# Kernel tuning notes

Hardware: AMD Instinct MI355X
Metric: run time of the kernel (lower is better)

The kernel has to match this reference:

```python
import jax, jax.numpy as jnp
import numpy as np

EPS = 1e-6
BASE_THETA = 10000.0


def setup_inputs() -> dict:
    key = jax.random.key(0)
    ks = jax.random.split(key, 6)
    S, E = 4096, 4096
    scale = 1.0 / np.sqrt(E)
    return {
        "x": jax.random.normal(ks[0], (S, E), dtype=jnp.float32),
        "w_q": jax.random.normal(ks[1], (E, E), dtype=jnp.float32) * scale,
        "w_k": jax.random.normal(ks[2], (E, E), dtype=jnp.float32) * scale,
        "w_v": jax.random.normal(ks[3], (E, E), dtype=jnp.float32) * scale,
        "w_out": jax.random.normal(ks[4], (E, E), dtype=jnp.float32) * scale,
        "scaling_factor": jax.random.uniform(ks[5], (E,), dtype=jnp.float32, minval=0.5, maxval=1.5),
    }


def _rope_apply(t, cos, sin):
    # t: (S, D) fp16; cos/sin: (S, D//2) fp16. Closed form of the per-position
    # block-diagonal 2x2 rotation matrix matmul in the original loop:
    # out[2j]   =  t[2j]*cos + t[2j+1]*sin
    # out[2j+1] = -t[2j]*sin + t[2j+1]*cos
    S, D = t.shape
    t2 = t.reshape(S, D // 2, 2)
    even, odd = t2[..., 0], t2[..., 1]
    out = jnp.stack([even * cos + odd * sin, -even * sin + odd * cos], axis=-1)
    return out.reshape(S, D)


def reference(x, w_q, w_k, w_v, w_out, scaling_factor):
    f16, f32 = jnp.float16, jnp.float32
    S, E = x.shape
    # __init__: q / q_inv / head rotations are identity; quantize = cast fp16 (scale 1).
    # q_inv * scaling_factor.view(1,-1) == diag(scaling_factor) -> row-scale weights.
    wq = (scaling_factor[:, None] * w_q).astype(f16)
    wk = (scaling_factor[:, None] * w_k).astype(f16)
    wv = (scaling_factor[:, None] * w_v).astype(f16)
    wo = w_out.astype(f16)

    # input @ identity; rms_norm in fp32
    xn = x * jax.lax.rsqrt(jnp.mean(x * x, axis=-1, keepdims=True) + EPS)
    xq = xn.astype(f16)

    # quantized matmuls: fp16 operands, fp32 accumulation, cast back to fp16
    q = (xq.astype(f32) @ wq.astype(f32)).astype(f16)
    k = (xq.astype(f32) @ wk.astype(f32)).astype(f16)
    v = (xq.astype(f32) @ wv.astype(f32)).astype(f16)

    # RoPE over full feature dim (size = E), vectorized over positions
    pos = jnp.arange(S, dtype=f32)[:, None]
    j = jnp.arange(E // 2, dtype=f32)[None, :]
    theta = pos / jnp.power(BASE_THETA, 2.0 * j / E)
    cos = jnp.cos(theta).astype(f16)
    sin = jnp.sin(theta).astype(f16)
    q = _rope_apply(q, cos, sin)
    k = _rope_apply(k, cos, sin)

    # rot_head_k_tiled is identity -> quantize is just fp16 cast (already fp16)
    scores = (q.astype(f32) @ k.T.astype(f32)).astype(f16)
    scores = scores / np.float16(np.sqrt(E))
    # causal mask: strict upper triangle -> -inf
    row = jnp.arange(S)[:, None]
    col = jnp.arange(S)[None, :]
    scores = jnp.where(col > row, jnp.float16(-jnp.inf), scores)
    attn_w = jax.nn.softmax(scores, axis=1)
    attn = attn_w @ v  # fp16 matmul as in original

    out = (attn.astype(f32) @ wo.astype(f32)).astype(f16)
    return out
```

## Files before the change

kernel.cpp:

```cpp
#include <hip/hip_runtime.h>
#include <hip/hip_bf16.h>
#include <cmath>


typedef _Float16 f16;
typedef _Float16 f16x4 __attribute__((ext_vector_type(4)));
typedef _Float16 f16x8 __attribute__((ext_vector_type(8)));
typedef float f32x4 __attribute__((ext_vector_type(4)));

#define S_DIM 4096
#define E_DIM 4096

__device__ __forceinline__ void gload_lds16(const void* g, void* l) {
  __builtin_amdgcn_global_load_lds((const __attribute__((address_space(1))) void*)g,
                                   (__attribute__((address_space(3))) void*)l,
                                   16, 0, 0);
}

__global__ __launch_bounds__(256) void rmsnorm_f16(const float* __restrict__ x,
                                                   f16* __restrict__ xq,
                                                   float* __restrict__ ftab,
                                                   int E) {
  const int row = blockIdx.x;
  const int t = threadIdx.x;
  if (row < 8) {
    const int j = row * 256 + t;
    ftab[j] = (float)pow(10000.0, (double)j / 2048.0);
  }
  const float4* xr = (const float4*)(x + (size_t)row * E);
  float4 v[4];
  float ss = 0.f;
#pragma unroll
  for (int i = 0; i < 4; ++i) {
    v[i] = xr[t + 256 * i];
    ss += v[i].x * v[i].x + v[i].y * v[i].y + v[i].z * v[i].z + v[i].w * v[i].w;
  }
#pragma unroll
  for (int o = 1; o < 64; o <<= 1) ss += __shfl_xor(ss, o);
  __shared__ float red[4];
  const int wid = t >> 6, lane = t & 63;
  if (lane == 0) red[wid] = ss;
  __syncthreads();
  const float tot = red[0] + red[1] + red[2] + red[3];
  const float r = 1.0f / sqrtf(tot / (float)E + 1e-6f);
  f16* xo = xq + (size_t)row * E;
#pragma unroll
  for (int i = 0; i < 4; ++i) {
    f16x4 o;
    o[0] = (f16)(v[i].x * r);
    o[1] = (f16)(v[i].y * r);
    o[2] = (f16)(v[i].z * r);
    o[3] = (f16)(v[i].w * r);
    *(f16x4*)(xo + 4 * (t + 256 * i)) = o;
  }
}

__global__ __launch_bounds__(256) void wconv_t(const float* __restrict__ W,
                                               const float* __restrict__ s,
                                               f16* __restrict__ WT, int N) {
  __shared__ f16 tile[64][65];
  const int tr = blockIdx.y * 64;
  const int tc = blockIdx.x * 64;
  const int t = threadIdx.x;
  const int r = t / 16;
  const int c4 = (t % 16) * 4;
#pragma unroll
  for (int i = 0; i < 4; ++i) {
    const int row = r + i * 16;
    float4 w = *(const float4*)(W + (size_t)(tr + row) * N + tc + c4);
    const float sc = s ? s[tr + row] : 1.0f;
    tile[row][c4 + 0] = (f16)(w.x * sc);
    tile[row][c4 + 1] = (f16)(w.y * sc);
    tile[row][c4 + 2] = (f16)(w.z * sc);
    tile[row][c4 + 3] = (f16)(w.w * sc);
  }
  __syncthreads();
#pragma unroll
  for (int i = 0; i < 4; ++i) {
    const int row = r + i * 16;
    f16x4 o;
    o[0] = tile[c4 + 0][row];
    o[1] = tile[c4 + 1][row];
    o[2] = tile[c4 + 2][row];
    o[3] = tile[c4 + 3][row];
    *(f16x4*)(WT + (size_t)(tc + row) * N + tr + c4) = o;
  }
}

__global__ __launch_bounds__(256) void rope_qk(f16* __restrict__ q,
                                               f16* __restrict__ k,
                                               const float* __restrict__ ftab,
                                               int E) {
  const int idx = blockIdx.x * 256 + threadIdx.x;
  const int cpr = E / 8;
  const int pos = idx / cpr;
  const int ch = idx % cpr;
  const int j0 = ch * 4;
  const float fpos = (float)pos;
  f16x8 qv = *(f16x8*)(q + (size_t)idx * 8);
  f16x8 kv = *(f16x8*)(k + (size_t)idx * 8);
  f16x8 qo, ko;
#pragma unroll
  for (int p = 0; p < 4; ++p) {
    const int j = j0 + p;
    const float th = fpos / ftab[j];
    float sn, cs;
    sincosf(th, &sn, &cs);
    const f16 c16 = (f16)cs, s16 = (f16)sn;
    const float c = (float)c16, s = (float)s16;
    {
      const float e = (float)qv[2 * p], o = (float)qv[2 * p + 1];
      const f16 t1 = (f16)(e * c), t2 = (f16)(o * s);
      const f16 u1 = (f16)(-(e * s)), u2 = (f16)(o * c);
      qo[2 * p] = (f16)((float)t1 + (float)t2);
      qo[2 * p + 1] = (f16)((float)u1 + (float)u2);
    }
    {
      const float e = (float)kv[2 * p], o = (float)kv[2 * p + 1];
      const f16 t1 = (f16)(e * c), t2 = (f16)(o * s);
      const f16 u1 = (f16)(-(e * s)), u2 = (f16)(o * c);
      ko[2 * p] = (f16)((float)t1 + (float)t2);
      ko[2 * p + 1] = (f16)((float)u1 + (float)u2);
    }
  }
  *(f16x8*)(q + (size_t)idx * 8) = qo;
  *(f16x8*)(k + (size_t)idx * 8) = ko;
}

__global__ __launch_bounds__(256) void softmax_causal(f16* __restrict__ sc, int S) {
  const int row = blockIdx.x;
  const int t = threadIdx.x;
  f16* p = sc + (size_t)row * S;
  const int cend = (row & ~255) + 256;
  float v[16];
  bool msk[16];
  bool act[2];
#pragma unroll
  for (int i = 0; i < 2; ++i) {
    act[i] = ((i * 256 + t) * 8) < cend;
    if (act[i]) {
      f16x8 a = *(const f16x8*)(p + (size_t)(i * 256 + t) * 8);
#pragma unroll
      for (int j = 0; j < 8; ++j) v[i * 8 + j] = (float)a[j];
    }
  }
  float m = -1e30f;
#pragma unroll
  for (int i = 0; i < 2; ++i)
    if (act[i])
#pragma unroll
      for (int j = 0; j < 8; ++j) {
        const int col = (i * 256 + t) * 8 + j;
        const int ii = i * 8 + j;
        msk[ii] = (col > row);
        if (!msk[ii]) m = fmaxf(m, v[ii]);
      }
#pragma unroll
  for (int o = 1; o < 64; o <<= 1) m = fmaxf(m, __shfl_xor(m, o));
  __shared__ float red[4];
  const int wid = t >> 6, lane = t & 63;
  if (lane == 0) red[wid] = m;
  __syncthreads();
  m = fmaxf(fmaxf(red[0], red[1]), fmaxf(red[2], red[3]));
  __syncthreads();
  f16 e16[16];
  float sum = 0.f;
#pragma unroll
  for (int i = 0; i < 2; ++i)
    if (act[i])
#pragma unroll
      for (int j = 0; j < 8; ++j) {
        const int ii = i * 8 + j;
        if (msk[ii]) {
          e16[ii] = (f16)0.0f;
        } else {
          const f16 d16 = (f16)(v[ii] - m);
          e16[ii] = (f16)expf((float)d16);
          sum += (float)e16[ii];
        }
      }
#pragma unroll
  for (int o = 1; o < 64; o <<= 1) sum += __shfl_xor(sum, o);
  if (lane == 0) red[wid] = sum;
  __syncthreads();
  sum = red[0] + red[1] + red[2] + red[3];
  const f16 den16 = (f16)sum;
  const float den = (float)den16;
#pragma unroll
  for (int i = 0; i < 2; ++i) {
    if (!act[i]) continue;
    f16x8 o;
#pragma unroll
    for (int j = 0; j < 8; ++j) {
      const int ii = i * 8 + j;
      o[j] = msk[ii] ? (f16)0.0f : (f16)((float)e16[ii] / den);
    }
    *(f16x8*)(p + (size_t)(i * 256 + t) * 8) = o;
  }
}

__device__ __forceinline__ void store_out(f16* p, f16 v) { *p = v; }
__device__ __forceinline__ void store_out(float* p, f16 v) { *p = (float)v; }

template <typename OUT, int MODE>
__global__ __launch_bounds__(512, 2) void gemm256(const f16* __restrict__ A,
                                                  const f16* __restrict__ BT,
                                                  OUT* __restrict__ C,
                                                  int M, int N, int K, float alpha) {
  if (MODE == 1 && blockIdx.x > blockIdx.y) return;
  const int bm = blockIdx.y * 256, bn = blockIdx.x * 256;
  const int kend = (MODE == 2) ? (bm + 256 < K ? bm + 256 : K) : K;
  const int nt = kend >> 6;

  extern __shared__ char smem[];
  f16(*lds)[2][256][64] = (f16(*)[2][256][64])smem;

  const int tid = threadIdx.x;
  const int lane = tid & 63;
  const int wid = tid >> 6;
  const int wr = wid >> 2;
  const int wc = wid & 3;
  const f16* Ab = A + (size_t)bm * K;
  const f16* Bb = BT + (size_t)bn * K;

  const int l8 = lane >> 3;
  const int gxor8 = ((lane & 7) ^ l8) * 8;
  const int lr = lane & 15;
  const int shi = lane >> 4;
  const int rsw = lr & 7;

  auto STAGE_P = [&](int p) {
    const int c = p + 6;
    const int Ts = c >> 2, hh = c & 3;
    if (Ts >= nt) return;
    const int k0 = Ts << 6;
    const int bsel = Ts & 1;
#pragma unroll
    for (int l = 0; l < 2; ++l) {
      const int rih0 = wid * 16 + l * 8;
      if (hh == 0 || hh == 3) {
        const int row0 = (rih0 & 63) + ((rih0 >> 6) << 7) + ((hh == 3) ? 64 : 0);
        gload_lds16(Ab + (size_t)(row0 + l8) * K + k0 + gxor8,
                    &lds[bsel][0][row0][0]);
      } else {
        const int row0 = (rih0 & 31) + ((rih0 >> 5) << 6) + ((hh == 2) ? 32 : 0);
        gload_lds16(Bb + (size_t)(row0 + l8) * K + k0 + gxor8,
                    &lds[bsel][1][row0][0]);
      }
    }
  };

  f32x4 acc[8][4] = {};
  f16x8 afr0[4][2], afr1[4][2], b0r[2][2], b1r[2][2];

#pragma unroll
  for (int p = -6; p < 0; ++p) STAGE_P(p);

  for (int T = 0; T < nt; ++T) {
    const int cur = T & 1;
    __builtin_amdgcn_sched_barrier(0);
    if (T + 1 < nt) {
      asm volatile("s_waitcnt vmcnt(4)" ::: "memory");
    } else {
      asm volatile("s_waitcnt vmcnt(0)" ::: "memory");
    }
    __builtin_amdgcn_sched_barrier(0);
    __builtin_amdgcn_s_barrier();
    __builtin_amdgcn_sched_barrier(0);
#pragma unroll
    for (int m2 = 0; m2 < 4; ++m2)
#pragma unroll
      for (int kk = 0; kk < 2; ++kk)
        afr0[m2][kk] = *(const f16x8*)&lds[cur][0][wr * 128 + m2 * 16 + lr]
                                          [((kk * 4 + shi) ^ rsw) * 8];
#pragma unroll
    for (int n2 = 0; n2 < 2; ++n2)
#pragma unroll
      for (int kk = 0; kk < 2; ++kk)
        b0r[n2][kk] = *(const f16x8*)&lds[cur][1][wc * 64 + n2 * 16 + lr]
                                         [((kk * 4 + shi) ^ rsw) * 8];
    STAGE_P(4 * T);
    __builtin_amdgcn_sched_barrier(0);
    if (T > 0) {
#pragma unroll
      for (int m2 = 0; m2 < 4; ++m2)
#pragma unroll
        for (int n2 = 0; n2 < 2; ++n2)
#pragma unroll
          for (int kk = 0; kk < 2; ++kk)
            acc[4 + m2][2 + n2] = __builtin_amdgcn_mfma_f32_16x16x32_f16(
                afr1[m2][kk], b1r[n2][kk], acc[4 + m2][2 + n2], 0, 0, 0);
    }
    __builtin_amdgcn_sched_barrier(0);
#pragma unroll
    for (int n2 = 0; n2 < 2; ++n2)
#pragma unroll
      for (int kk = 0; kk < 2; ++kk)
        b1r[n2][kk] = *(const f16x8*)&lds[cur][1][wc * 64 + 32 + n2 * 16 + lr]
                                         [((kk * 4 + shi) ^ rsw) * 8];
    STAGE_P(4 * T + 1);
    __builtin_amdgcn_sched_barrier(0);
#pragma unroll
    for (int m2 = 0; m2 < 4; ++m2)
#pragma unroll
      for (int n2 = 0; n2 < 2; ++n2)
#pragma unroll
        for (int kk = 0; kk < 2; ++kk)
          acc[m2][n2] = __builtin_amdgcn_mfma_f32_16x16x32_f16(
              afr0[m2][kk], b0r[n2][kk], acc[m2][n2], 0, 0, 0);
    __builtin_amdgcn_sched_barrier(0);
    __builtin_amdgcn_s_barrier();
    __builtin_amdgcn_sched_barrier(0);
#pragma unroll
    for (int m2 = 0; m2 < 4; ++m2)
#pragma unroll
      for (int kk = 0; kk < 2; ++kk)
        afr1[m2][kk] = *(const f16x8*)&lds[cur][0][wr * 128 + 64 + m2 * 16 + lr]
                                          [((kk * 4 + shi) ^ rsw) * 8];
    STAGE_P(4 * T + 2);
    __builtin_amdgcn_sched_barrier(0);
#pragma unroll
    for (int m2 = 0; m2 < 4; ++m2)
#pragma unroll
      for (int n2 = 0; n2 < 2; ++n2)
#pragma unroll
        for (int kk = 0; kk < 2; ++kk)
          acc[m2][2 + n2] = __builtin_amdgcn_mfma_f32_16x16x32_f16(
              afr0[m2][kk], b1r[n2][kk], acc[m2][2 + n2], 0, 0, 0);
    __builtin_amdgcn_sched_barrier(0);
    STAGE_P(4 * T + 3);
    __builtin_amdgcn_sched_barrier(0);
#pragma unroll
    for (int m2 = 0; m2 < 4; ++m2)
#pragma unroll
      for (int n2 = 0; n2 < 2; ++n2)
#pragma unroll
        for (int kk = 0; kk < 2; ++kk)
          acc[4 + m2][n2] = __builtin_amdgcn_mfma_f32_16x16x32_f16(
              afr1[m2][kk], b0r[n2][kk], acc[4 + m2][n2], 0, 0, 0);
  }
#pragma unroll
  for (int m2 = 0; m2 < 4; ++m2)
#pragma unroll
    for (int n2 = 0; n2 < 2; ++n2)
#pragma unroll
      for (int kk = 0; kk < 2; ++kk)
        acc[4 + m2][2 + n2] = __builtin_amdgcn_mfma_f32_16x16x32_f16(
            afr1[m2][kk], b1r[n2][kk], acc[4 + m2][2 + n2], 0, 0, 0);

  const int rb_l = wr * 128 + (lane >> 4) * 4;
  const int cb_l = wc * 64 + (lane & 15);

#pragma unroll
  for (int mm = 0; mm < 8; ++mm)
#pragma unroll
    for (int nn = 0; nn < 4; ++nn) {
      const int col = bn + cb_l + nn * 16;
#pragma unroll
      for (int r = 0; r < 4; ++r) {
        f16 h = (f16)acc[mm][nn][r];
        if (alpha != 1.0f) h = (f16)((float)h * alpha);
        store_out(&C[(size_t)(bm + rb_l + mm * 16 + r) * N + col], h);
      }
    }
}

extern "C" void kernel_launch(void* const* d_in, const int* in_sizes, int n_in,
                              void* d_out, int out_size, void* d_ws, size_t ws_size,
                              hipStream_t stream) {
  const float* x = (const float*)d_in[0];
  const float* wq = (const float*)d_in[1];
  const float* wk = (const float*)d_in[2];
  const float* wv = (const float*)d_in[3];
  const float* wo = (const float*)d_in[4];
  const float* sf = (const float*)d_in[5];
  float* out = (float*)d_out;

  const int S = S_DIM, E = E_DIM;
  const size_t U = (size_t)S * E * sizeof(f16);
  char* ws = (char*)d_ws;
  f16* xq = (f16*)(ws + 0 * U);
  f16* wT = (f16*)(ws + 1 * U);
  f16* q  = (f16*)(ws + 2 * U);
  f16* k  = (f16*)(ws + 3 * U);
  f16* vT = (f16*)d_out;
  float* ftab = out + 12 * 1024 * 1024;

  const int LDSA = 131072;
  hipFuncSetAttribute(reinterpret_cast<const void*>(&gemm256<f16, 0>),
                      hipFuncAttributeMaxDynamicSharedMemorySize, LDSA);
  hipFuncSetAttribute(reinterpret_cast<const void*>(&gemm256<f16, 1>),
                      hipFuncAttributeMaxDynamicSharedMemorySize, LDSA);
  hipFuncSetAttribute(reinterpret_cast<const void*>(&gemm256<f16, 2>),
                      hipFuncAttributeMaxDynamicSharedMemorySize, LDSA);
  hipFuncSetAttribute(reinterpret_cast<const void*>(&gemm256<float, 0>),
                      hipFuncAttributeMaxDynamicSharedMemorySize, LDSA);

  dim3 b256(256), b512(512);
  dim3 gT(E / 64, E / 64);
  dim3 gG(E / 256, S / 256);

  rmsnorm_f16<<<S, b256, 0, stream>>>(x, xq, ftab, E);

  wconv_t<<<gT, b256, 0, stream>>>(wq, sf, wT, E);
  gemm256<f16, 0><<<gG, b512, LDSA, stream>>>(xq, wT, q, S, E, E, 1.0f);
  wconv_t<<<gT, b256, 0, stream>>>(wk, sf, wT, E);
  gemm256<f16, 0><<<gG, b512, LDSA, stream>>>(xq, wT, k, S, E, E, 1.0f);
  wconv_t<<<gT, b256, 0, stream>>>(wv, sf, wT, E);
  gemm256<f16, 0><<<dim3(S / 256, E / 256), b512, LDSA, stream>>>(wT, xq, vT,
                                                                  E, S, E, 1.0f);

  rope_qk<<<(S * (E / 8)) / 256, b256, 0, stream>>>(q, k, ftab, E);

  f16* sc = wT;
  gemm256<f16, 1><<<dim3(S / 256, S / 256), b512, LDSA, stream>>>(q, k, sc, S, S,
                                                                  E, 1.0f / 64.0f);
  softmax_causal<<<S, b256, 0, stream>>>(sc, S);

  f16* attn = q;
  gemm256<f16, 2><<<gG, b512, LDSA, stream>>>(sc, vT, attn, S, E, S, 1.0f);

  f16* wT2 = k;
  wconv_t<<<gT, b256, 0, stream>>>(wo, (const float*)nullptr, wT2, E);
  gemm256<float, 0><<<gG, b512, LDSA, stream>>>(attn, wT2, out, S, E, E, 1.0f);
}
```

Measured before the change: 779.3 us.

## Use 128x128 tile GEMM kernel for causal QK^T and PV matmuls

Adds a simpler 128x128-tile GEMM kernel with 256 threads and static LDS, and uses it for the causal score GEMM and the attention-times-V GEMM. The causal block-skipping and K-truncation now operate at 128 granularity, and the softmax column bound is tightened to match. This trims wasted work above the diagonal and improves tile-count balance. The trade-off is that the new kernel is single-buffered with less data reuse than the tuned 256 kernel.

```diff
diff --git a/kernel.cpp b/kernel.cpp
--- a/kernel.cpp
+++ b/kernel.cpp
@@ -131,7 +131,7 @@
   const int row = blockIdx.x;
   const int t = threadIdx.x;
   f16* p = sc + (size_t)row * S;
-  const int cend = (row & ~255) + 256;
+  const int cend = (row & ~127) + 128;
   float v[16];
   bool msk[16];
   bool act[2];
@@ -202,15 +202,82 @@
 __device__ __forceinline__ void store_out(f16* p, f16 v) { *p = v; }
 __device__ __forceinline__ void store_out(float* p, f16 v) { *p = (float)v; }
 
-template <typename OUT, int MODE>
+template <int MODE>
+__global__ __launch_bounds__(256) void gemm128(const f16* __restrict__ A,
+                                               const f16* __restrict__ BT,
+                                               f16* __restrict__ C,
+                                               int M, int N, int K, float alpha) {
+  const int bm = blockIdx.y * 128, bn = blockIdx.x * 128;
+  if (MODE == 1 && bn > bm) return;
+  const int kend = (MODE == 2) ? (bm + 128 < K ? bm + 128 : K) : K;
+
+  __shared__ f16 As[128][64];
+  __shared__ f16 Bs[128][64];
+  const int t = threadIdx.x;
+  const int lane = t & 63;
+  const int wid = t >> 6;
+  const int wr = wid >> 1, wc = wid & 1;
+
+  const int lr = lane & 15;
+  const int shi = lane >> 4;
+  const int rx = lr & 7;
+  const int grow = wid * 8 + (lane >> 3);
+  const int gcol = (((lane & 7) ^ ((lane >> 3) & 7)) * 8);
+
+  f32x4 acc[4][4] = {};
+
+  for (int k0 = 0; k0 < kend; k0 += 64) {
+    __syncthreads();
+#pragma unroll
+    for (int i = 0; i < 4; ++i) {
+      gload_lds16(A + (size_t)(bm + i * 32 + grow) * K + k0 + gcol,
+                  &As[i * 32 + wid * 8][0]);
+      gload_lds16(BT + (size_t)(bn + i * 32 + grow) * K + k0 + gcol,
+                  &Bs[i * 32 + wid * 8][0]);
+    }
+    __syncthreads();
+#pragma unroll
+    for (int kk = 0; kk < 2; ++kk) {
+      const int roff = ((kk * 4 + shi) ^ rx) * 8;
+      f16x8 af[4], bf[4];
+#pragma unroll
+      for (int m = 0; m < 4; ++m)
+        af[m] = *(const f16x8*)&As[wr * 64 + m * 16 + lr][roff];
+#pragma unroll
+      for (int n = 0; n < 4; ++n)
+        bf[n] = *(const f16x8*)&Bs[wc * 64 + n * 16 + lr][roff];
+#pragma unroll
+      for (int m = 0; m < 4; ++m)
+#pragma unroll
+        for (int n = 0; n < 4; ++n)
+          acc[m][n] =
+              __builtin_amdgcn_mfma_f32_16x16x32_f16(af[m], bf[n], acc[m][n], 0, 0, 0);
+    }
+  }
+
+  const int rb = bm + wr * 64 + (lane >> 4) * 4;
+  const int cb = bn + wc * 64 + (lane & 15);
+#pragma unroll
+  for (int m = 0; m < 4; ++m)
+#pragma unroll
+    for (int n = 0; n < 4; ++n) {
+      const int col = cb + n * 16;
+#pragma unroll
+      for (int r = 0; r < 4; ++r) {
+        f16 h = (f16)acc[m][n][r];
+        if (alpha != 1.0f) h = (f16)((float)h * alpha);
+        store_out(&C[(size_t)(rb + m * 16 + r) * N + col], h);
+      }
+    }
+}
+
+template <typename OUT>
 __global__ __launch_bounds__(512, 2) void gemm256(const f16* __restrict__ A,
                                                   const f16* __restrict__ BT,
                                                   OUT* __restrict__ C,
                                                   int M, int N, int K, float alpha) {
-  if (MODE == 1 && blockIdx.x > blockIdx.y) return;
   const int bm = blockIdx.y * 256, bn = blockIdx.x * 256;
-  const int kend = (MODE == 2) ? (bm + 256 < K ? bm + 256 : K) : K;
-  const int nt = kend >> 6;
+  const int nt = K >> 6;
 
   extern __shared__ char smem[];
   f16(*lds)[2][256][64] = (f16(*)[2][256][64])smem;
@@ -387,13 +454,9 @@
   float* ftab = out + 12 * 1024 * 1024;
 
   const int LDSA = 131072;
-  hipFuncSetAttribute(reinterpret_cast<const void*>(&gemm256<f16, 0>),
+  hipFuncSetAttribute(reinterpret_cast<const void*>(&gemm256<f16>),
                       hipFuncAttributeMaxDynamicSharedMemorySize, LDSA);
-  hipFuncSetAttribute(reinterpret_cast<const void*>(&gemm256<f16, 1>),
-                      hipFuncAttributeMaxDynamicSharedMemorySize, LDSA);
-  hipFuncSetAttribute(reinterpret_cast<const void*>(&gemm256<f16, 2>),
-                      hipFuncAttributeMaxDynamicSharedMemorySize, LDSA);
-  hipFuncSetAttribute(reinterpret_cast<const void*>(&gemm256<float, 0>),
+  hipFuncSetAttribute(reinterpret_cast<const void*>(&gemm256<float>),
                       hipFuncAttributeMaxDynamicSharedMemorySize, LDSA);
 
   dim3 b256(256), b512(512);
@@ -403,24 +466,25 @@
   rmsnorm_f16<<<S, b256, 0, stream>>>(x, xq, ftab, E);
 
   wconv_t<<<gT, b256, 0, stream>>>(wq, sf, wT, E);
-  gemm256<f16, 0><<<gG, b512, LDSA, stream>>>(xq, wT, q, S, E, E, 1.0f);
+  gemm256<f16><<<gG, b512, LDSA, stream>>>(xq, wT, q, S, E, E, 1.0f);
   wconv_t<<<gT, b256, 0, stream>>>(wk, sf, wT, E);
-  gemm256<f16, 0><<<gG, b512, LDSA, stream>>>(xq, wT, k, S, E, E, 1.0f);
+  gemm256<f16><<<gG, b512, LDSA, stream>>>(xq, wT, k, S, E, E, 1.0f);
   wconv_t<<<gT, b256, 0, stream>>>(wv, sf, wT, E);
-  gemm256<f16, 0><<<dim3(S / 256, E / 256), b512, LDSA, stream>>>(wT, xq, vT,
-                                                                  E, S, E, 1.0f);
+  gemm256<f16><<<dim3(S / 256, E / 256), b512, LDSA, stream>>>(wT, xq, vT,
+                                                               E, S, E, 1.0f);
 
   rope_qk<<<(S * (E / 8)) / 256, b256, 0, stream>>>(q, k, ftab, E);
 
   f16* sc = wT;
-  gemm256<f16, 1><<<dim3(S / 256, S / 256), b512, LDSA, stream>>>(q, k, sc, S, S,
-                                                                  E, 1.0f / 64.0f);
+  gemm128<1><<<dim3(S / 128, S / 128), b256, 0, stream>>>(q, k, sc, S, S, E,
+                                                          1.0f / 64.0f);
   softmax_causal<<<S, b256, 0, stream>>>(sc, S);
 
   f16* attn = q;
-  gemm256<f16, 2><<<gG, b512, LDSA, stream>>>(sc, vT, attn, S, E, S, 1.0f);
+  gemm128<2><<<dim3(E / 128, S / 128), b256, 0, stream>>>(sc, vT, attn, S, E, S,
+                                                          1.0f);
 
   f16* wT2 = k;
   wconv_t<<<gT, b256, 0, stream>>>(wo, (const float*)nullptr, wT2, E);
-  gemm256<float, 0><<<gG, b512, LDSA, stream>>>(attn, wT2, out, S, E, E, 1.0f);
-}
+  gemm256<float><<<gG, b512, LDSA, stream>>>(attn, wT2, out, S, E, E, 1.0f);
+}
```

Result: slower. 837.9 us (+7.5%).
